# Kernel optimization log

Measured on AMD Instinct MI355X. Metric: run time of the kernel, lower is better.

Reference implementation:

```python
import jax, jax.numpy as jnp
import numpy as np
from jax import lax

NUM_CLASSES = 80
INPUT_SIZE = 416.0
CONF_THR = 0.5
IOU_THR = 0.5
# Standard YOLOv3 COCO anchors; anchors[3*idx:3*idx+3] pairs large anchors with 13x13 head.
ANCHORS = np.array([[116, 90], [156, 198], [373, 326],
                    [30, 61], [62, 45], [59, 119],
                    [10, 13], [16, 30], [33, 23]], dtype=np.float32)


def setup_inputs() -> dict:
    key = jax.random.key(0)
    k0, k1, k2 = jax.random.split(key, 3)
    C = 3 * (5 + NUM_CLASSES)  # 255
    return {
        "p0": jax.random.normal(k0, (1, C, 13, 13), dtype=jnp.float32),
        "p1": jax.random.normal(k1, (1, C, 26, 26), dtype=jnp.float32),
        "p2": jax.random.normal(k2, (1, C, 52, 52), dtype=jnp.float32),
    }


def _decode(pred, anchors):
    # pred: [B, na*(5+nc), H, W]; anchors: [na, 2] in input_size scale
    b, _, lh, lw = pred.shape
    na = anchors.shape[0]
    stride_w = INPUT_SIZE / lw
    stride_h = INPUT_SIZE / lh
    scaled_anchors = anchors / jnp.array([stride_w, stride_h], dtype=pred.dtype)  # [na,2]
    p = pred.reshape(b, na, 5 + NUM_CLASSES, lh, lw).transpose(0, 1, 3, 4, 2)  # [b,na,h,w,ch]
    gx, gy = jnp.meshgrid(jnp.arange(lw, dtype=pred.dtype),
                          jnp.arange(lh, dtype=pred.dtype), indexing='xy')
    grid = jnp.stack([gx, gy], axis=-1)  # [h,w,2], grid[h,w]=(w,h)
    pxy = jax.nn.sigmoid(p[..., 0:2]) + grid  # broadcast over b,na
    pwh = jnp.exp(p[..., 2:4]) * scaled_anchors[None, :, None, None, :]
    stride = jnp.array([stride_w, stride_h, stride_w, stride_h], dtype=pred.dtype)
    pbox = jnp.concatenate([pxy, pwh], axis=-1).reshape(b, -1, 4) * stride
    pconf = jax.nn.sigmoid(p[..., 4]).reshape(b, -1)
    # argmax over sigmoid(logits) == argmax over logits (monotonic)
    pcls = jnp.argmax(p[..., 5:], axis=-1).reshape(b, -1)
    return pbox, pconf, pcls


def _nms(boxes, conf, cls):
    # boxes: [N,4] (cx,cy,w,h), conf: [N], cls: [N] int
    N = boxes.shape[0]
    valid = conf >= CONF_THR
    score = jnp.where(valid, conf, -1.0)
    order = jnp.argsort(-score)  # descending confidence, invalid at the end
    b = boxes[order]
    v = valid[order]
    c = cls[order]
    s = conf[order]
    # corners
    half = b[:, 2:4] * 0.5
    x1y1 = b[:, 0:2] - half
    x2y2 = b[:, 0:2] + half
    area = b[:, 2] * b[:, 3]
    # pairwise IoU [N,N] (dominant, memory-bound intermediate)
    lt = jnp.maximum(x1y1[:, None, :], x1y1[None, :, :])
    rb = jnp.minimum(x2y2[:, None, :], x2y2[None, :, :])
    wh = jnp.clip(rb - lt, 0.0)
    inter = wh[..., 0] * wh[..., 1]
    union = area[:, None] + area[None, :] - inter
    iou = inter / jnp.maximum(union, 1e-9)
    same_cls = c[:, None] == c[None, :]
    sup_cand = same_cls & (iou > IOU_THR)  # candidate suppressors
    idx = jnp.arange(N)

    def body(i, keep):
        suppressed = jnp.any(keep & (idx < i) & sup_cand[i])
        return keep.at[i].set(v[i] & jnp.logical_not(suppressed))

    keep = lax.fori_loop(0, N, body, jnp.zeros((N,), dtype=bool))
    out = jnp.concatenate([b, s[:, None], c.astype(b.dtype)[:, None]], axis=-1)
    return jnp.where(keep[:, None], out, 0.0)


def reference(p0, p1, p2):
    preds = [p0, p1, p2]
    boxes, confs, clss = [], [], []
    for i, p in enumerate(preds):
        anc = jnp.asarray(ANCHORS[3 * i:3 * i + 3])
        pb, pc, pk = _decode(p, anc)
        boxes.append(pb)
        confs.append(pc)
        clss.append(pk)
    boxes = jnp.concatenate(boxes, axis=1)[0]   # [10647,4]
    conf = jnp.concatenate(confs, axis=1)[0]    # [10647]
    cls = jnp.concatenate(clss, axis=1)[0]      # [10647]
    return _nms(boxes, conf, cls)
```

## Files before the change

kernel.cpp:

```cpp
#include <hip/hip_runtime.h>
#include <stdint.h>

#define N_TOT 10647
#define NB    42
#define NBD   167
#define NCLS  80
#define BCAP  320
#define WPB   5

typedef unsigned long long ull;

#define G_CNT  0
#define G_V    NCLS

__constant__ float c_aw[9] = {116.f,156.f,373.f, 30.f,62.f,59.f, 10.f,16.f,33.f};
__constant__ float c_ah[9] = { 90.f,198.f,326.f, 61.f,45.f,119.f, 13.f,30.f,23.f};

__device__ __forceinline__ float sigmoidf_(float x) { return 1.0f / (1.0f + expf(-x)); }

__global__ void __launch_bounds__(256)
decode_kernel(const float* __restrict__ p0, const float* __restrict__ p1,
              const float* __restrict__ p2,
              float* __restrict__ box, float* __restrict__ conf,
              float* __restrict__ score, int* __restrict__ cls,
              int* __restrict__ rank)
{
    __shared__ float sbest[4][64];
    __shared__ int   sbi[4][64];
    int sub  = threadIdx.x >> 6;
    int lane = threadIdx.x & 63;
    int n = blockIdx.x * 64 + lane;
    bool inb = (n < N_TOT);
    const float* p; int H, base, lvl; float stride;
    int nn = inb ? n : 0;
    if (nn < 507)       { p = p0; H = 13; base = 0;    stride = 32.f; lvl = 0; }
    else if (nn < 2535) { p = p1; H = 26; base = 507;  stride = 16.f; lvl = 1; }
    else                { p = p2; H = 52; base = 2535; stride = 8.f;  lvl = 2; }
    int m   = nn - base;
    int HW  = H * H;
    int a   = m / HW;
    int rem = m - a * HW;
    const float* q = p + (size_t)(a * 85) * HW + rem;
    float best = -3.4e38f; int bi = 20 * sub;
    if (inb) {
        int c0 = 20 * sub;
        #pragma unroll 5
        for (int c = c0; c < c0 + 20; ++c) {
            float v = q[(size_t)(5 + c) * HW];
            if (v > best) { best = v; bi = c; }
        }
    }
    sbest[sub][lane] = best;
    sbi[sub][lane]   = bi;
    __syncthreads();
    if (sub == 0 && inb) {
        rank[n] = 0;
        float b0 = sbest[0][lane]; int i0 = sbi[0][lane];
        #pragma unroll
        for (int s = 1; s < 4; ++s) {
            float bs = sbest[s][lane];
            if (bs > b0) { b0 = bs; i0 = sbi[s][lane]; }
        }
        int gy = rem / H;
        int gx = rem - gy * H;
        float tx = q[0];
        float ty = q[(size_t)HW];
        float tw = q[(size_t)2*HW];
        float th = q[(size_t)3*HW];
        float tc = q[(size_t)4*HW];
        float cx = (sigmoidf_(tx) + (float)gx) * stride;
        float cy = (sigmoidf_(ty) + (float)gy) * stride;
        float bw = expf(tw) * c_aw[lvl*3 + a];
        float bh = expf(th) * c_ah[lvl*3 + a];
        float cf = sigmoidf_(tc);
        box[n*4+0] = cx; box[n*4+1] = cy; box[n*4+2] = bw; box[n*4+3] = bh;
        conf[n] = cf;
        cls[n]  = i0;
        score[n] = (cf >= 0.5f) ? cf : -1.0f;
    }
}

__global__ void __launch_bounds__(256)
rank_partial_kernel(const float* __restrict__ score, int* __restrict__ rank,
                    int* __restrict__ gctr)
{
    __shared__ float tile[256];
    int tid = threadIdx.x;
    if (blockIdx.x == 0 && blockIdx.y == 0 && tid <= NCLS) gctr[tid] = 0;
    int i   = blockIdx.x * 256 + tid;
    int j0  = blockIdx.y * 256;
    int jj  = j0 + tid;
    tile[tid] = (jj < N_TOT) ? score[jj] : -2.0f;
    __syncthreads();
    float si = (i < N_TOT) ? score[i] : -2.0f;
    if (i >= N_TOT || si < 0.0f) return;
    int r = 0;
    #pragma unroll 8
    for (int t = 0; t < 256; ++t) {
        float sj = tile[t];
        r += (sj > si || (sj == si && (j0 + t) < i)) ? 1 : 0;
    }
    if (r) atomicAdd(&rank[i], r);
}

__global__ void __launch_bounds__(256)
bucket_kernel(const float* __restrict__ score, const float* __restrict__ box,
              const float* __restrict__ conf, const int* __restrict__ cls,
              const int* __restrict__ rank, int* __restrict__ gctr,
              float4* __restrict__ cbox4, float* __restrict__ cconf,
              int* __restrict__ crank)
{
    __shared__ int s_cnt;
    const int tid = threadIdx.x;
    if (tid == 0) s_cnt = 0;
    __syncthreads();
    int i = blockIdx.x * 256 + tid;
    if (i < N_TOT && score[i] >= 0.0f) {
        int c = cls[i];
        int pos = atomicAdd(&gctr[G_CNT + c], 1);
        if (pos < BCAP) {
            cbox4[c * BCAP + pos] = *(const float4*)&box[i * 4];
            cconf[c * BCAP + pos] = conf[i];
            crank[c * BCAP + pos] = rank[i];
        }
        atomicAdd(&s_cnt, 1);
    }
    __syncthreads();
    if (tid == 0 && s_cnt) atomicAdd(&gctr[G_V], s_cnt);
}

__global__ void __launch_bounds__(256)
class_nms_kernel(const float4* __restrict__ cbox4, const float* __restrict__ cconf,
                 const int* __restrict__ crank, const int* __restrict__ gctr,
                 float* __restrict__ out)
{
    __shared__ float bcx[BCAP], bcy[BCAP], bw_[BCAP], bh_[BCAP], bcf[BCAP];
    __shared__ uint16_t brank[BCAP];
    __shared__ ull smask[BCAP][WPB];
    __shared__ ull keepm[WPB], nxtm[WPB];
    __shared__ int s_changed;
    const int c   = blockIdx.x;
    const int tid = threadIdx.x;
    const int n   = min(gctr[G_CNT + c], BCAP);
    const int V   = gctr[G_V];
    for (int a = tid; a < n; a += 256) {
        float4 b4 = cbox4[c * BCAP + a];
        bcx[a] = b4.x; bcy[a] = b4.y; bw_[a] = b4.z; bh_[a] = b4.w;
        bcf[a] = cconf[c * BCAP + a];
        brank[a] = (uint16_t)crank[c * BCAP + a];
    }
    __syncthreads();
    for (int a = tid; a < n; a += 256) {
        float ax1 = bcx[a] - bw_[a]*0.5f, ay1 = bcy[a] - bh_[a]*0.5f;
        float ax2 = bcx[a] + bw_[a]*0.5f, ay2 = bcy[a] + bh_[a]*0.5f;
        float aar = bw_[a] * bh_[a];
        int ra = brank[a];
        ull msk[WPB] = {0,0,0,0,0};
        for (int b = 0; b < n; ++b) {
            if (b == a) continue;
            if (brank[b] >= ra) continue;
            float bx1 = bcx[b] - bw_[b]*0.5f, by1 = bcy[b] - bh_[b]*0.5f;
            float bx2 = bcx[b] + bw_[b]*0.5f, by2 = bcy[b] + bh_[b]*0.5f;
            float xx1 = fmaxf(ax1, bx1);
            float yy1 = fmaxf(ay1, by1);
            float xx2 = fminf(ax2, bx2);
            float yy2 = fminf(ay2, by2);
            float w = fmaxf(xx2 - xx1, 0.0f);
            float h = fmaxf(yy2 - yy1, 0.0f);
            float inter = w * h;
            float uni   = aar + bw_[b]*bh_[b] - inter;
            float iou   = inter / fmaxf(uni, 1e-9f);
            if (iou > 0.5f) msk[b >> 6] |= (1ull << (b & 63));
        }
        #pragma unroll
        for (int w = 0; w < WPB; ++w) smask[a][w] = msk[w];
    }
    if (tid < WPB) {
        int rem = n - (tid << 6);
        keepm[tid] = (rem >= 64) ? ~0ull : ((rem > 0) ? ((1ull << rem) - 1ull) : 0ull);
    }
    __syncthreads();
    for (int round = 0; round <= n + 2 && n > 0; ++round) {
        if (tid < WPB) nxtm[tid] = 0ull;
        if (tid == 0) s_changed = 0;
        __syncthreads();
        for (int a = tid; a < n; a += 256) {
            ull sup = 0ull;
            #pragma unroll
            for (int w = 0; w < WPB; ++w) sup |= (smask[a][w] & keepm[w]);
            if (sup == 0ull) atomicOr(&nxtm[a >> 6], 1ull << (a & 63));
        }
        __syncthreads();
        if (tid < WPB) {
            if (nxtm[tid] != keepm[tid]) { s_changed = 1; keepm[tid] = nxtm[tid]; }
        }
        __syncthreads();
        if (!s_changed) break;
        __syncthreads();
    }
    for (int a = tid; a < n; a += 256) {
        int r = brank[a];
        bool kept = (keepm[a >> 6] >> (a & 63)) & 1ull;
        float v0=0.f,v1=0.f,v2=0.f,v3=0.f,v4=0.f,v5=0.f;
        if (kept) {
            v0 = bcx[a]; v1 = bcy[a]; v2 = bw_[a]; v3 = bh_[a];
            v4 = bcf[a]; v5 = (float)c;
        }
        out[r*6+0]=v0; out[r*6+1]=v1; out[r*6+2]=v2;
        out[r*6+3]=v3; out[r*6+4]=v4; out[r*6+5]=v5;
    }
    int tail  = N_TOT - V;
    int chunk = (tail + NCLS - 1) / NCLS;
    int rbeg  = V + c * chunk;
    int rend  = min(rbeg + chunk, N_TOT);
    for (int r = rbeg + tid; r < rend; r += 256) {
        out[r*6+0]=0.f; out[r*6+1]=0.f; out[r*6+2]=0.f;
        out[r*6+3]=0.f; out[r*6+4]=0.f; out[r*6+5]=0.f;
    }
}

extern "C" void kernel_launch(void* const* d_in, const int* in_sizes, int n_in,
                              void* d_out, int out_size, void* d_ws, size_t ws_size,
                              hipStream_t stream) {
    const float* p0 = (const float*)d_in[0];
    const float* p1 = (const float*)d_in[1];
    const float* p2 = (const float*)d_in[2];
    float* out = (float*)d_out;
    char* ws = (char*)d_ws;
    const int N = N_TOT;

    float* box   = (float*)ws;
    float* conf  = box + 4*N;
    float* score = conf + N;
    int* cls   = (int*)(score + N);
    int* rank  = cls + N;
    int* gctr  = rank + N;
    float4* cbox4 = (float4*)(((uintptr_t)(gctr + NCLS + 1) + 15) & ~(uintptr_t)15);
    float*  cconf = (float*)(cbox4 + NCLS * BCAP);
    int*    crank = (int*)(cconf + NCLS * BCAP);

    decode_kernel<<<NBD, 256, 0, stream>>>(p0, p1, p2, box, conf, score, cls, rank);
    rank_partial_kernel<<<dim3(NB, NB), 256, 0, stream>>>(score, rank, gctr);
    bucket_kernel<<<NB, 256, 0, stream>>>(score, box, conf, cls, rank, gctr,
                                          cbox4, cconf, crank);
    class_nms_kernel<<<NCLS, 256, 0, stream>>>(cbox4, cconf, crank, gctr, out);
}
```

Baseline: 56.24 us.

## Fuse rank and bucket kernels into one launch, store indices instead of ranks

Merges the rank-counting pass and the class-bucketing pass into a single grid with an extra row of blocks that does bucketing. Because bucketing no longer waits for final ranks, buckets store the original detection index, and the NMS kernel gathers the rank through it. The gctr reset moves into the decode kernel. This removes one kernel launch and its inter-kernel gap, at the cost of an indirect rank gather in the NMS load.

```diff
diff --git a/kernel.cpp b/kernel.cpp
--- a/kernel.cpp
+++ b/kernel.cpp
@@ -23,10 +23,11 @@
               const float* __restrict__ p2,
               float* __restrict__ box, float* __restrict__ conf,
               float* __restrict__ score, int* __restrict__ cls,
-              int* __restrict__ rank)
+              int* __restrict__ rank, int* __restrict__ gctr)
 {
     __shared__ float sbest[4][64];
     __shared__ int   sbi[4][64];
+    if (blockIdx.x == 0 && threadIdx.x <= NCLS) gctr[threadIdx.x] = 0;
     int sub  = threadIdx.x >> 6;
     int lane = threadIdx.x & 63;
     int n = blockIdx.x * 64 + lane;
@@ -81,58 +82,53 @@
 }
 
 __global__ void __launch_bounds__(256)
-rank_partial_kernel(const float* __restrict__ score, int* __restrict__ rank,
-                    int* __restrict__ gctr)
+rank_bucket_kernel(const float* __restrict__ score, const float* __restrict__ box,
+                   const float* __restrict__ conf, const int* __restrict__ cls,
+                   int* __restrict__ rank, int* __restrict__ gctr,
+                   float4* __restrict__ cbox4, float* __restrict__ cconf,
+                   int* __restrict__ cidx)
 {
     __shared__ float tile[256];
-    int tid = threadIdx.x;
-    if (blockIdx.x == 0 && blockIdx.y == 0 && tid <= NCLS) gctr[tid] = 0;
-    int i   = blockIdx.x * 256 + tid;
-    int j0  = blockIdx.y * 256;
-    int jj  = j0 + tid;
-    tile[tid] = (jj < N_TOT) ? score[jj] : -2.0f;
-    __syncthreads();
-    float si = (i < N_TOT) ? score[i] : -2.0f;
-    if (i >= N_TOT || si < 0.0f) return;
-    int r = 0;
-    #pragma unroll 8
-    for (int t = 0; t < 256; ++t) {
-        float sj = tile[t];
-        r += (sj > si || (sj == si && (j0 + t) < i)) ? 1 : 0;
-    }
-    if (r) atomicAdd(&rank[i], r);
-}
-
-__global__ void __launch_bounds__(256)
-bucket_kernel(const float* __restrict__ score, const float* __restrict__ box,
-              const float* __restrict__ conf, const int* __restrict__ cls,
-              const int* __restrict__ rank, int* __restrict__ gctr,
-              float4* __restrict__ cbox4, float* __restrict__ cconf,
-              int* __restrict__ crank)
-{
     __shared__ int s_cnt;
     const int tid = threadIdx.x;
-    if (tid == 0) s_cnt = 0;
-    __syncthreads();
-    int i = blockIdx.x * 256 + tid;
-    if (i < N_TOT && score[i] >= 0.0f) {
-        int c = cls[i];
-        int pos = atomicAdd(&gctr[G_CNT + c], 1);
-        if (pos < BCAP) {
-            cbox4[c * BCAP + pos] = *(const float4*)&box[i * 4];
-            cconf[c * BCAP + pos] = conf[i];
-            crank[c * BCAP + pos] = rank[i];
-        }
-        atomicAdd(&s_cnt, 1);
-    }
-    __syncthreads();
-    if (tid == 0 && s_cnt) atomicAdd(&gctr[G_V], s_cnt);
+    if (blockIdx.y < NB) {
+        int i   = blockIdx.x * 256 + tid;
+        int j0  = blockIdx.y * 256;
+        int jj  = j0 + tid;
+        tile[tid] = (jj < N_TOT) ? score[jj] : -2.0f;
+        __syncthreads();
+        float si = (i < N_TOT) ? score[i] : -2.0f;
+        if (i >= N_TOT || si < 0.0f) return;
+        int r = 0;
+        #pragma unroll 8
+        for (int t = 0; t < 256; ++t) {
+            float sj = tile[t];
+            r += (sj > si || (sj == si && (j0 + t) < i)) ? 1 : 0;
+        }
+        if (r) atomicAdd(&rank[i], r);
+    } else {
+        if (tid == 0) s_cnt = 0;
+        __syncthreads();
+        int i = blockIdx.x * 256 + tid;
+        if (i < N_TOT && score[i] >= 0.0f) {
+            int c = cls[i];
+            int pos = atomicAdd(&gctr[G_CNT + c], 1);
+            if (pos < BCAP) {
+                cbox4[c * BCAP + pos] = *(const float4*)&box[i * 4];
+                cconf[c * BCAP + pos] = conf[i];
+                cidx[c * BCAP + pos]  = i;
+            }
+            atomicAdd(&s_cnt, 1);
+        }
+        __syncthreads();
+        if (tid == 0 && s_cnt) atomicAdd(&gctr[G_V], s_cnt);
+    }
 }
 
 __global__ void __launch_bounds__(256)
 class_nms_kernel(const float4* __restrict__ cbox4, const float* __restrict__ cconf,
-                 const int* __restrict__ crank, const int* __restrict__ gctr,
-                 float* __restrict__ out)
+                 const int* __restrict__ cidx, const int* __restrict__ rank,
+                 const int* __restrict__ gctr, float* __restrict__ out)
 {
     __shared__ float bcx[BCAP], bcy[BCAP], bw_[BCAP], bh_[BCAP], bcf[BCAP];
     __shared__ uint16_t brank[BCAP];
@@ -147,7 +143,7 @@
         float4 b4 = cbox4[c * BCAP + a];
         bcx[a] = b4.x; bcy[a] = b4.y; bw_[a] = b4.z; bh_[a] = b4.w;
         bcf[a] = cconf[c * BCAP + a];
-        brank[a] = (uint16_t)crank[c * BCAP + a];
+        brank[a] = (uint16_t)rank[cidx[c * BCAP + a]];
     }
     __syncthreads();
     for (int a = tid; a < n; a += 256) {
@@ -237,11 +233,10 @@
     int* gctr  = rank + N;
     float4* cbox4 = (float4*)(((uintptr_t)(gctr + NCLS + 1) + 15) & ~(uintptr_t)15);
     float*  cconf = (float*)(cbox4 + NCLS * BCAP);
-    int*    crank = (int*)(cconf + NCLS * BCAP);
-
-    decode_kernel<<<NBD, 256, 0, stream>>>(p0, p1, p2, box, conf, score, cls, rank);
-    rank_partial_kernel<<<dim3(NB, NB), 256, 0, stream>>>(score, rank, gctr);
-    bucket_kernel<<<NB, 256, 0, stream>>>(score, box, conf, cls, rank, gctr,
-                                          cbox4, cconf, crank);
-    class_nms_kernel<<<NCLS, 256, 0, stream>>>(cbox4, cconf, crank, gctr, out);
-}
+    int*    cidx  = (int*)(cconf + NCLS * BCAP);
+
+    decode_kernel<<<NBD, 256, 0, stream>>>(p0, p1, p2, box, conf, score, cls, rank, gctr);
+    rank_bucket_kernel<<<dim3(NB, NB + 1), 256, 0, stream>>>(score, box, conf, cls,
+                                                             rank, gctr, cbox4, cconf, cidx);
+    class_nms_kernel<<<NCLS, 256, 0, stream>>>(cbox4, cconf, cidx, rank, gctr, out);
+}
```

Result: faster. 46.91 us, median of 2 (-16.6%).
